# Kernel tuning notes

Measured on AMD Instinct MI355X. Metric: run time of the kernel, lower is better.

Reference implementation:

```python
import jax, jax.numpy as jnp
from jax import lax
import numpy as np

B, C_IN, H, W = 256, 2, 15, 15
DIM_MID, DIM_OUT = 128, 64
N_RES = 4  # DirectionalConvResBlocks

# tap positions inside a 3x3 kernel for each of the 4 line directions
# (matches DirectionalConvLayer.weight_func_map: horiz, vert, diag, anti-diag)
_POS = (((1, 0), (1, 1), (1, 2)),
        ((0, 1), (1, 1), (2, 1)),
        ((0, 0), (1, 1), (2, 2)),
        ((2, 0), (1, 1), (0, 2)))


def _dir_kernel(w3, d):
    # w3: [3, O, I] -> [O, I, 3, 3] with taps placed along direction d
    O, I = w3.shape[1], w3.shape[2]
    kern = jnp.zeros((O, I, 3, 3), w3.dtype)
    for k, (r, c) in enumerate(_POS[d]):
        kern = kern.at[:, :, r, c].set(w3[k])
    return kern


def _dconv(x, w3, b, d):
    kern = _dir_kernel(w3, d)
    y = lax.conv_general_dilated(x, kern, window_strides=(1, 1),
                                 padding=((1, 1), (1, 1)),
                                 dimension_numbers=('NCHW', 'OIHW', 'NCHW'))
    return y + b[None, :, None, None]


def _pw(x, w, b):
    # 1x1 conv: w [O, I]
    return jnp.einsum('bihw,oi->bohw', x, w) + b[None, :, None, None]


def setup_inputs() -> dict:
    key = jax.random.key(0)
    ks = jax.random.split(key, 16)
    s_in = 1.0 / np.sqrt(3 * C_IN)
    s_mid = 1.0 / np.sqrt(3 * DIM_MID)
    s_pw = 1.0 / np.sqrt(DIM_MID)
    return {
        'x': jax.random.normal(ks[0], (B, C_IN, H, W), jnp.float32),
        'dconv0_w': jax.random.normal(ks[1], (3, DIM_MID, C_IN), jnp.float32) * s_in,
        'dconv0_b': jnp.zeros((DIM_MID,), jnp.float32),
        'rb_dconv_w': jax.random.normal(ks[2], (N_RES, 3, DIM_MID, DIM_MID), jnp.float32) * s_mid,
        'rb_dconv_b': jnp.zeros((N_RES, DIM_MID), jnp.float32),
        'rb_c1_w': jax.random.normal(ks[3], (N_RES, DIM_MID, DIM_MID), jnp.float32) * s_pw,
        'rb_c1_b': jnp.zeros((N_RES, DIM_MID), jnp.float32),
        'c0_w1': jax.random.normal(ks[4], (DIM_MID, DIM_MID), jnp.float32) * s_pw,
        'c0_b1': jnp.zeros((DIM_MID,), jnp.float32),
        'c0_w2': jax.random.normal(ks[5], (DIM_MID, DIM_MID), jnp.float32) * s_pw,
        'c0_b2': jnp.zeros((DIM_MID,), jnp.float32),
        'final_w': jax.random.normal(ks[6], (DIM_OUT, DIM_MID), jnp.float32) * s_pw,
        'final_b': jnp.zeros((DIM_OUT,), jnp.float32),
    }


def reference(x, dconv0_w, dconv0_b, rb_dconv_w, rb_dconv_b, rb_c1_w, rb_c1_b,
              c0_w1, c0_b1, c0_w2, c0_b2, final_w, final_b):
    silu = jax.nn.silu
    outs = []
    for d in range(4):  # 4 board directions, shared weights
        h = silu(_dconv(x, dconv0_w, dconv0_b, d))
        for i in range(N_RES):  # DirectionalConvResBlock
            r = h
            h = silu(_dconv(h, rb_dconv_w[i], rb_dconv_b[i], d))
            h = silu(_pw(h, rb_c1_w[i], rb_c1_b[i]))
            h = h + r
        # Conv0dResBlock
        r = h
        h = silu(_pw(h, c0_w1, c0_b1))
        h = silu(_pw(h, c0_w2, c0_b2))
        h = h + r
        outs.append(_pw(h, final_w, final_b))
    return jnp.stack(outs, axis=1)  # [B, 4, DIM_OUT, H, W]
```

## Files before the change

kernel.cpp:

```cpp
#include <hip/hip_runtime.h>
#include <cstdint>
#include <cstddef>


#define HWX 15
#define NPOS 225
#define CH 128
#define NTH 256
#define ABYTES 8192
#define HOFF ABYTES
#define GRID_SLOTS 273
#define LDS_BYTES (ABYTES + GRID_SLOTS*256)
#define SAFE_PP 136

#define WSE_WDC 0
#define WSE_WC1 196608
#define WSE_W01 262144
#define WSE_W02 278528
#define WSE_WF  294912
#define WSE_TOTAL 303104
#define WS_NEED (WSE_TOTAL*2)

typedef _Float16 f16;
typedef __attribute__((ext_vector_type(8))) _Float16 f16x8;
typedef __attribute__((ext_vector_type(4))) _Float16 f16x4;
typedef __attribute__((ext_vector_type(4))) float f32x4;

__device__ __forceinline__ int hb_addr(int pp, int k){
  return HOFF + pp*256 + ((k*2) ^ ((pp&15)<<4));
}
__device__ __forceinline__ int a_addr(int o, int k){
  return o*64 + ((((k>>3))<<4) ^ ((o&3)<<4)) + ((k&7)*2);
}
__device__ __forceinline__ float silu_f(float v){ return v / (1.f + __expf(-v)); }

struct StReg { f16x8 a, b; bool on; };

template<bool WS>
__device__ __forceinline__ StReg stage_load(const f16* __restrict__ wsblk,
                                            const float* __restrict__ f32p,
                                            int stride, int rows, int tid){
  StReg r;
  const int o = tid>>1, kh = tid&1;
  r.on = (o < rows);
  if (r.on){
    if (WS){
      r.a = *(const f16x8*)(wsblk + o*32 + kh*16);
      r.b = *(const f16x8*)(wsblk + o*32 + kh*16 + 8);
    } else {
      const float* s = f32p + (size_t)o*stride + kh*16;
      float4 x0 = *(const float4*)(s);
      float4 x1 = *(const float4*)(s+4);
      float4 x2 = *(const float4*)(s+8);
      float4 x3 = *(const float4*)(s+12);
      r.a = (f16x8){(f16)x0.x,(f16)x0.y,(f16)x0.z,(f16)x0.w,
                    (f16)x1.x,(f16)x1.y,(f16)x1.z,(f16)x1.w};
      r.b = (f16x8){(f16)x2.x,(f16)x2.y,(f16)x2.z,(f16)x2.w,
                    (f16)x3.x,(f16)x3.y,(f16)x3.z,(f16)x3.w};
    }
  }
  return r;
}

__device__ __forceinline__ void stage_write(char* sm, StReg r, int tid){
  const int o = tid>>1, kh = tid&1;
  if (r.on){
    *(f16x8*)(sm + a_addr(o, kh*16))   = r.a;
    *(f16x8*)(sm + a_addr(o, kh*16+8)) = r.b;
  }
}

template<int MT>
__device__ __forceinline__ void gemm32(const char* sm, const int* pbs, int ks,
                                       int krow, int col, f32x4 acc[4][8]){
  const int kb = ks + krow*8;
  const int ka = krow*8;
  f16x8 b0 = *(const f16x8*)(sm + hb_addr(pbs[0], kb));
  f16x8 b1 = *(const f16x8*)(sm + hb_addr(pbs[1], kb));
  f16x8 b2 = *(const f16x8*)(sm + hb_addr(pbs[2], kb));
  f16x8 b3 = *(const f16x8*)(sm + hb_addr(pbs[3], kb));
#pragma unroll
  for (int mt=0; mt<MT; mt++){
    f16x8 a = *(const f16x8*)(sm + a_addr(mt*16+col, ka));
    acc[0][mt] = __builtin_amdgcn_mfma_f32_16x16x32_f16(a, b0, acc[0][mt], 0,0,0);
    acc[1][mt] = __builtin_amdgcn_mfma_f32_16x16x32_f16(a, b1, acc[1][mt], 0,0,0);
    acc[2][mt] = __builtin_amdgcn_mfma_f32_16x16x32_f16(a, b2, acc[2][mt], 0,0,0);
    acc[3][mt] = __builtin_amdgcn_mfma_f32_16x16x32_f16(a, b3, acc[3][mt], 0,0,0);
  }
}

template<int MT, bool WS>
__device__ __forceinline__ void pw_pass(char* sm, const f16* __restrict__ wsblk,
                                        const float* __restrict__ f32p,
                                        int stride, int rows, const int* pbs,
                                        int krow, int col, int tid, f32x4 acc[4][8]){
  StReg cur = stage_load<WS>(wsblk, f32p, stride, rows, tid);
#pragma unroll 1
  for (int ks=0; ks<CH; ks+=32){
    __syncthreads();
    stage_write(sm, cur, tid);
    if (ks+32 < CH)
      cur = stage_load<WS>(wsblk + (ks/32+1)*rows*32, f32p + ks + 32, stride, rows, tid);
    __syncthreads();
    gemm32<MT>(sm, pbs, ks, krow, col, acc);
  }
}

__device__ __forceinline__ void zacc_all(f32x4 acc[4][8]){
#pragma unroll
  for (int t=0;t<4;t++)
#pragma unroll
    for (int m=0;m<8;m++) acc[t][m] = (f32x4){0.f,0.f,0.f,0.f};
}

__device__ __forceinline__ void snap4x8(const char* sm, f16x4 r[4][8],
                                        const int* pbs, int krow){
#pragma unroll
  for (int t=0;t<4;t++)
#pragma unroll
    for (int mt=0;mt<8;mt++)
      r[t][mt] = *(const f16x4*)(sm + hb_addr(pbs[t], mt*16 + krow*4));
}

template<int MT, bool SILU, bool RES>
__device__ __forceinline__ void wb4(char* sm, f32x4 acc[4][8],
                                    const float* __restrict__ bias,
                                    f16x4 rsd[4][8], const int* pbs,
                                    const bool* val, int krow){
#pragma unroll
  for (int mt=0;mt<MT;mt++){
    const int ch0 = mt*16 + krow*4;
    float4 bb = *(const float4*)(bias + ch0);
    const float bj[4] = {bb.x, bb.y, bb.z, bb.w};
#pragma unroll
    for (int t=0;t<4;t++){
      f32x4 v = acc[t][mt];
#pragma unroll
      for (int j=0;j<4;j++) v[j] += bj[j];
      if (SILU){
#pragma unroll
        for (int j=0;j<4;j++) v[j] = silu_f(v[j]);
      }
      if (RES){
        f16x4 r = rsd[t][mt];
#pragma unroll
        for (int j=0;j<4;j++) v[j] += (float)r[j];
      }
      if (val[t]){
        f16x4 o = { (f16)v[0],(f16)v[1],(f16)v[2],(f16)v[3] };
        *(f16x4*)(sm + hb_addr(pbs[t], ch0)) = o;
      }
    }
  }
}

struct P {
  const float *x, *w0, *b0, *wdc, *bdc, *wc1, *bc1, *w01, *b01, *w02, *b02, *wf, *bf;
};

template<bool WS>
__global__ __launch_bounds__(NTH, 2)
void mix9_v3(const P p, const f16* __restrict__ wsf, float* __restrict__ out)
{
  __shared__ char sm[LDS_BYTES];
  const int tid  = threadIdx.x;
  const int lane = tid & 63;
  const int wave = tid >> 6;
  const int col  = lane & 15;
  const int krow = lane >> 4;
  const int d = blockIdx.x & 3;
  const int b = blockIdx.x >> 2;

  for (int i = tid; i < LDS_BYTES/16; i += NTH)
    ((f32x4*)sm)[i] = (f32x4){0.f,0.f,0.f,0.f};
  __syncthreads();

  for (int i = tid; i < 2*NPOS; i += NTH){
    const int ic = i/NPOS, n = i%NPOS;
    const int pp = (n/HWX + 1)*16 + (n%HWX + 1);
    *(f16*)(sm + hb_addr(pp, ic)) = (f16)p.x[(size_t)b*2*NPOS + i];
  }

  int pbs[4]; bool val[4];
#pragma unroll
  for (int t=0;t<4;t++){
    const int r = wave*4 + t;
    val[t] = (col >= 1) && (r < HWX);
    pbs[t] = val[t] ? (r+1)*16 + col : SAFE_PP;
  }
  int dneg;
  switch (d){
    case 0:  dneg = -1;  break;
    case 1:  dneg = -16; break;
    case 2:  dneg = -17; break;
    default: dneg =  15; break;
  }

  f32x4 acc[4][8];
  f16x4 rsd[4][8];

  zacc_all(acc);
#pragma unroll 1
  for (int k=0;k<3;k++){
    const int sh = (k==0) ? dneg : (k==1) ? 0 : -dneg;
    int pbt[4];
#pragma unroll
    for (int t=0;t<4;t++) pbt[t] = pbs[t] + sh;
    __syncthreads();
    *(f16*)(sm + a_addr(tid>>1, tid&1)) = (f16)p.w0[k*256 + tid];
    __syncthreads();
    gemm32<8>(sm, pbt, 0, krow, col, acc);
  }
  __syncthreads();
  wb4<8,true,false>(sm, acc, p.b0, nullptr, pbs, val, krow);

#pragma unroll 1
  for (int res=0; res<4; res++){
    zacc_all(acc);
#pragma unroll 1
    for (int k=0;k<3;k++){
      const int sh = (k==0) ? dneg : (k==1) ? 0 : -dneg;
      int pbt[4];
#pragma unroll
      for (int t=0;t<4;t++) pbt[t] = pbs[t] + sh;
      const f16* blk = wsf + WSE_WDC + (size_t)(res*3 + k)*4*4096;
      const float* fp = p.wdc + (size_t)(res*3 + k)*CH*CH;
      pw_pass<8,WS>(sm, blk, fp, CH, CH, pbt, krow, col, tid, acc);
    }
    __syncthreads();
    snap4x8(sm, rsd, pbs, krow);
    wb4<8,true,false>(sm, acc, p.bdc + res*CH, nullptr, pbs, val, krow);

    zacc_all(acc);
    pw_pass<8,WS>(sm, wsf + WSE_WC1 + (size_t)res*4*4096,
                  p.wc1 + (size_t)res*CH*CH, CH, CH, pbs, krow, col, tid, acc);
    __syncthreads();
    wb4<8,true,true>(sm, acc, p.bc1 + res*CH, rsd, pbs, val, krow);
  }

  zacc_all(acc);
  pw_pass<8,WS>(sm, wsf + WSE_W01, p.w01, CH, CH, pbs, krow, col, tid, acc);
  __syncthreads();
  snap4x8(sm, rsd, pbs, krow);
  wb4<8,true,false>(sm, acc, p.b01, nullptr, pbs, val, krow);

  zacc_all(acc);
  pw_pass<8,WS>(sm, wsf + WSE_W02, p.w02, CH, CH, pbs, krow, col, tid, acc);
  __syncthreads();
  wb4<8,true,true>(sm, acc, p.b02, rsd, pbs, val, krow);

  zacc_all(acc);
  pw_pass<4,WS>(sm, wsf + WSE_WF, p.wf, CH, 64, pbs, krow, col, tid, acc);

  float* ob = out + ((size_t)(b*4 + d)*64)*NPOS;
#pragma unroll
  for (int t=0;t<4;t++){
    const int r = wave*4 + t;
    const int n = r*HWX + (col-1);
#pragma unroll
    for (int mt=0;mt<4;mt++){
      const int ch0 = mt*16 + krow*4;
      float4 bb = *(const float4*)(p.bf + ch0);
      const float bj[4] = {bb.x, bb.y, bb.z, bb.w};
#pragma unroll
      for (int j=0;j<4;j++)
        if (val[t]) ob[(size_t)(ch0+j)*NPOS + n] = acc[t][mt][j] + bj[j];
    }
  }
}

__global__ void cvt_ws(const P p, f16* __restrict__ ws)
{
  const int idx = blockIdx.x*NTH + threadIdx.x;
  if (idx >= WSE_TOTAL) return;
  float v;
  if (idx < WSE_WC1){
    int blk = idx >> 12, rem = idx & 4095;
    int o = rem >> 5, k = rem & 31;
    int ks = blk & 3, tapres = blk >> 2;
    v = p.wdc[((size_t)tapres*CH + o)*CH + ks*32 + k];
  } else if (idx < WSE_W01){
    int j = idx - WSE_WC1;
    int blk = j >> 12, rem = j & 4095;
    int o = rem >> 5, k = rem & 31;
    int ks = blk & 3, res = blk >> 2;
    v = p.wc1[((size_t)res*CH + o)*CH + ks*32 + k];
  } else if (idx < WSE_W02){
    int j = idx - WSE_W01;
    int ks = j >> 12, rem = j & 4095;
    int o = rem >> 5, k = rem & 31;
    v = p.w01[(size_t)o*CH + ks*32 + k];
  } else if (idx < WSE_WF){
    int j = idx - WSE_W02;
    int ks = j >> 12, rem = j & 4095;
    int o = rem >> 5, k = rem & 31;
    v = p.w02[(size_t)o*CH + ks*32 + k];
  } else {
    int j = idx - WSE_WF;
    int ks = j >> 11, rem = j & 2047;
    int o = rem >> 5, k = rem & 31;
    v = p.wf[(size_t)o*CH + ks*32 + k];
  }
  ws[idx] = (f16)v;
}

extern "C" void kernel_launch(void* const* d_in, const int* in_sizes, int n_in,
                              void* d_out, int out_size, void* d_ws, size_t ws_size,
                              hipStream_t stream)
{
  (void)in_sizes; (void)n_in; (void)out_size;
  P p;
  p.x   = (const float*)d_in[0];
  p.w0  = (const float*)d_in[1];
  p.b0  = (const float*)d_in[2];
  p.wdc = (const float*)d_in[3];
  p.bdc = (const float*)d_in[4];
  p.wc1 = (const float*)d_in[5];
  p.bc1 = (const float*)d_in[6];
  p.w01 = (const float*)d_in[7];
  p.b01 = (const float*)d_in[8];
  p.w02 = (const float*)d_in[9];
  p.b02 = (const float*)d_in[10];
  p.wf  = (const float*)d_in[11];
  p.bf  = (const float*)d_in[12];

  float* out = (float*)d_out;
  const bool ws_ok = (d_ws != nullptr) && (ws_size >= (size_t)WS_NEED);

  if (ws_ok){
    f16* ws = (f16*)d_ws;
    cvt_ws<<<dim3((WSE_TOTAL + NTH - 1)/NTH), dim3(NTH), 0, stream>>>(p, ws);
    mix9_v3<true><<<dim3(256*4), dim3(NTH), 0, stream>>>(p, ws, out);
  } else {
    mix9_v3<false><<<dim3(256*4), dim3(NTH), 0, stream>>>(p, nullptr, out);
  }
}
```

Before: 518.5 us.

## Load MFMA weight fragments directly from global memory instead of LDS staging

Drops the LDS A-operand staging buffer and the two barriers per k-slice. Each wave now reads its f16 weight fragments straight from the pre-converted workspace (L2/L1 cached) inside the MFMA loop. The first-layer weights are pre-packed into the workspace as zero-padded tiles, and output is staged through LDS so the global stores are coalesced float4 writes. This trades LDS traffic and barrier stalls for redundant global/cache loads across the four waves, and adds a few barriers around the writebacks.

After: 975.5 us. 1.88x slower.

```diff
diff --git a/kernel.cpp b/kernel.cpp
--- a/kernel.cpp
+++ b/kernel.cpp
@@ -7,10 +7,8 @@
 #define NPOS 225
 #define CH 128
 #define NTH 256
-#define ABYTES 8192
-#define HOFF ABYTES
 #define GRID_SLOTS 273
-#define LDS_BYTES (ABYTES + GRID_SLOTS*256)
+#define LDS_BYTES (GRID_SLOTS*256)
 #define SAFE_PP 136
 
 #define WSE_WDC 0
@@ -18,7 +16,8 @@
 #define WSE_W01 262144
 #define WSE_W02 278528
 #define WSE_WF  294912
-#define WSE_TOTAL 303104
+#define WSE_W0  303104
+#define WSE_TOTAL 315392
 #define WS_NEED (WSE_TOTAL*2)
 
 typedef _Float16 f16;
@@ -27,61 +26,32 @@
 typedef __attribute__((ext_vector_type(4))) float f32x4;
 
 __device__ __forceinline__ int hb_addr(int pp, int k){
-  return HOFF + pp*256 + ((k*2) ^ ((pp&15)<<4));
-}
-__device__ __forceinline__ int a_addr(int o, int k){
-  return o*64 + ((((k>>3))<<4) ^ ((o&3)<<4)) + ((k&7)*2);
+  return pp*256 + ((k*2) ^ ((pp&15)<<4));
 }
 __device__ __forceinline__ float silu_f(float v){ return v / (1.f + __expf(-v)); }
 
-struct StReg { f16x8 a, b; bool on; };
-
-template<bool WS>
-__device__ __forceinline__ StReg stage_load(const f16* __restrict__ wsblk,
-                                            const float* __restrict__ f32p,
-                                            int stride, int rows, int tid){
-  StReg r;
-  const int o = tid>>1, kh = tid&1;
-  r.on = (o < rows);
-  if (r.on){
+template<int MT, bool WS>
+__device__ __forceinline__ void gemm_k32(const char* sm, const f16* __restrict__ wsblk,
+    const float* __restrict__ f32w, const int* pbt, int ksabs, int krow, int col,
+    f32x4 acc[4][8]){
+  const int kb = ksabs + krow*8;
+  const int k8 = krow*8;
+  f16x8 b0 = *(const f16x8*)(sm + hb_addr(pbt[0], kb));
+  f16x8 b1 = *(const f16x8*)(sm + hb_addr(pbt[1], kb));
+  f16x8 b2 = *(const f16x8*)(sm + hb_addr(pbt[2], kb));
+  f16x8 b3 = *(const f16x8*)(sm + hb_addr(pbt[3], kb));
+#pragma unroll
+  for (int mt=0; mt<MT; mt++){
+    const int o = mt*16 + col;
+    f16x8 a;
     if (WS){
-      r.a = *(const f16x8*)(wsblk + o*32 + kh*16);
-      r.b = *(const f16x8*)(wsblk + o*32 + kh*16 + 8);
+      a = *(const f16x8*)(wsblk + o*32 + k8);
     } else {
-      const float* s = f32p + (size_t)o*stride + kh*16;
-      float4 x0 = *(const float4*)(s);
-      float4 x1 = *(const float4*)(s+4);
-      float4 x2 = *(const float4*)(s+8);
-      float4 x3 = *(const float4*)(s+12);
-      r.a = (f16x8){(f16)x0.x,(f16)x0.y,(f16)x0.z,(f16)x0.w,
-                    (f16)x1.x,(f16)x1.y,(f16)x1.z,(f16)x1.w};
-      r.b = (f16x8){(f16)x2.x,(f16)x2.y,(f16)x2.z,(f16)x2.w,
-                    (f16)x3.x,(f16)x3.y,(f16)x3.z,(f16)x3.w};
-    }
-  }
-  return r;
-}
-
-__device__ __forceinline__ void stage_write(char* sm, StReg r, int tid){
-  const int o = tid>>1, kh = tid&1;
-  if (r.on){
-    *(f16x8*)(sm + a_addr(o, kh*16))   = r.a;
-    *(f16x8*)(sm + a_addr(o, kh*16+8)) = r.b;
-  }
-}
-
-template<int MT>
-__device__ __forceinline__ void gemm32(const char* sm, const int* pbs, int ks,
-                                       int krow, int col, f32x4 acc[4][8]){
-  const int kb = ks + krow*8;
-  const int ka = krow*8;
-  f16x8 b0 = *(const f16x8*)(sm + hb_addr(pbs[0], kb));
-  f16x8 b1 = *(const f16x8*)(sm + hb_addr(pbs[1], kb));
-  f16x8 b2 = *(const f16x8*)(sm + hb_addr(pbs[2], kb));
-  f16x8 b3 = *(const f16x8*)(sm + hb_addr(pbs[3], kb));
-#pragma unroll
-  for (int mt=0; mt<MT; mt++){
-    f16x8 a = *(const f16x8*)(sm + a_addr(mt*16+col, ka));
+      const float* s = f32w + (size_t)o*CH + ksabs + k8;
+      float4 x0 = *(const float4*)(s), x1 = *(const float4*)(s+4);
+      a = (f16x8){(f16)x0.x,(f16)x0.y,(f16)x0.z,(f16)x0.w,
+                  (f16)x1.x,(f16)x1.y,(f16)x1.z,(f16)x1.w};
+    }
     acc[0][mt] = __builtin_amdgcn_mfma_f32_16x16x32_f16(a, b0, acc[0][mt], 0,0,0);
     acc[1][mt] = __builtin_amdgcn_mfma_f32_16x16x32_f16(a, b1, acc[1][mt], 0,0,0);
     acc[2][mt] = __builtin_amdgcn_mfma_f32_16x16x32_f16(a, b2, acc[2][mt], 0,0,0);
@@ -90,19 +60,39 @@
 }
 
 template<int MT, bool WS>
-__device__ __forceinline__ void pw_pass(char* sm, const f16* __restrict__ wsblk,
-                                        const float* __restrict__ f32p,
-                                        int stride, int rows, const int* pbs,
-                                        int krow, int col, int tid, f32x4 acc[4][8]){
-  StReg cur = stage_load<WS>(wsblk, f32p, stride, rows, tid);
-#pragma unroll 1
-  for (int ks=0; ks<CH; ks+=32){
-    __syncthreads();
-    stage_write(sm, cur, tid);
-    if (ks+32 < CH)
-      cur = stage_load<WS>(wsblk + (ks/32+1)*rows*32, f32p + ks + 32, stride, rows, tid);
-    __syncthreads();
-    gemm32<MT>(sm, pbs, ks, krow, col, acc);
+__device__ __forceinline__ void pass128(const char* sm, const f16* __restrict__ wsbase,
+    int blkElems, const float* __restrict__ f32w, const int* pbt, int krow, int col,
+    f32x4 acc[4][8]){
+#pragma unroll
+  for (int kq=0; kq<4; kq++)
+    gemm_k32<MT,WS>(sm, wsbase + (size_t)kq*blkElems, f32w, pbt, kq*32, krow, col, acc);
+}
+
+template<bool WS>
+__device__ __forceinline__ void gemm_l0(const char* sm, const f16* __restrict__ wsblk,
+    const float* __restrict__ w0tap, const int* pbt, int krow, int col, f32x4 acc[4][8]){
+  const int kb = krow*8;
+  f16x8 b0 = *(const f16x8*)(sm + hb_addr(pbt[0], kb));
+  f16x8 b1 = *(const f16x8*)(sm + hb_addr(pbt[1], kb));
+  f16x8 b2 = *(const f16x8*)(sm + hb_addr(pbt[2], kb));
+  f16x8 b3 = *(const f16x8*)(sm + hb_addr(pbt[3], kb));
+#pragma unroll
+  for (int mt=0; mt<8; mt++){
+    const int o = mt*16 + col;
+    f16x8 a;
+    if (WS){
+      a = *(const f16x8*)(wsblk + o*32 + kb);
+    } else {
+      a = (f16x8){(f16)0,(f16)0,(f16)0,(f16)0,(f16)0,(f16)0,(f16)0,(f16)0};
+      if (krow == 0){
+        float2 w = *(const float2*)(w0tap + o*2);
+        a[0] = (f16)w.x; a[1] = (f16)w.y;
+      }
+    }
+    acc[0][mt] = __builtin_amdgcn_mfma_f32_16x16x32_f16(a, b0, acc[0][mt], 0,0,0);
+    acc[1][mt] = __builtin_amdgcn_mfma_f32_16x16x32_f16(a, b1, acc[1][mt], 0,0,0);
+    acc[2][mt] = __builtin_amdgcn_mfma_f32_16x16x32_f16(a, b2, acc[2][mt], 0,0,0);
+    acc[3][mt] = __builtin_amdgcn_mfma_f32_16x16x32_f16(a, b3, acc[3][mt], 0,0,0);
   }
 }
 
@@ -160,7 +150,7 @@
 
 template<bool WS>
 __global__ __launch_bounds__(NTH, 2)
-void mix9_v3(const P p, const f16* __restrict__ wsf, float* __restrict__ out)
+void mix9_v4(const P p, const f16* __restrict__ wsf, float* __restrict__ out)
 {
   __shared__ char sm[LDS_BYTES];
   const int tid  = threadIdx.x;
@@ -180,6 +170,7 @@
     const int pp = (n/HWX + 1)*16 + (n%HWX + 1);
     *(f16*)(sm + hb_addr(pp, ic)) = (f16)p.x[(size_t)b*2*NPOS + i];
   }
+  __syncthreads();
 
   int pbs[4]; bool val[4];
 #pragma unroll
@@ -206,13 +197,12 @@
     int pbt[4];
 #pragma unroll
     for (int t=0;t<4;t++) pbt[t] = pbs[t] + sh;
-    __syncthreads();
-    *(f16*)(sm + a_addr(tid>>1, tid&1)) = (f16)p.w0[k*256 + tid];
-    __syncthreads();
-    gemm32<8>(sm, pbt, 0, krow, col, acc);
+    gemm_l0<WS>(sm, wsf + WSE_W0 + (size_t)k*4096, p.w0 + (size_t)k*CH*2,
+                pbt, krow, col, acc);
   }
   __syncthreads();
   wb4<8,true,false>(sm, acc, p.b0, nullptr, pbs, val, krow);
+  __syncthreads();
 
 #pragma unroll 1
   for (int res=0; res<4; res++){
@@ -223,50 +213,60 @@
       int pbt[4];
 #pragma unroll
       for (int t=0;t<4;t++) pbt[t] = pbs[t] + sh;
-      const f16* blk = wsf + WSE_WDC + (size_t)(res*3 + k)*4*4096;
-      const float* fp = p.wdc + (size_t)(res*3 + k)*CH*CH;
-      pw_pass<8,WS>(sm, blk, fp, CH, CH, pbt, krow, col, tid, acc);
+      pass128<8,WS>(sm, wsf + WSE_WDC + (size_t)(res*3+k)*4*4096, 4096,
+                    p.wdc + (size_t)(res*3+k)*CH*CH, pbt, krow, col, acc);
     }
     __syncthreads();
     snap4x8(sm, rsd, pbs, krow);
     wb4<8,true,false>(sm, acc, p.bdc + res*CH, nullptr, pbs, val, krow);
+    __syncthreads();
 
     zacc_all(acc);
-    pw_pass<8,WS>(sm, wsf + WSE_WC1 + (size_t)res*4*4096,
-                  p.wc1 + (size_t)res*CH*CH, CH, CH, pbs, krow, col, tid, acc);
+    pass128<8,WS>(sm, wsf + WSE_WC1 + (size_t)res*4*4096, 4096,
+                  p.wc1 + (size_t)res*CH*CH, pbs, krow, col, acc);
     __syncthreads();
     wb4<8,true,true>(sm, acc, p.bc1 + res*CH, rsd, pbs, val, krow);
+    __syncthreads();
   }
 
   zacc_all(acc);
-  pw_pass<8,WS>(sm, wsf + WSE_W01, p.w01, CH, CH, pbs, krow, col, tid, acc);
+  pass128<8,WS>(sm, wsf + WSE_W01, 4096, p.w01, pbs, krow, col, acc);
   __syncthreads();
   snap4x8(sm, rsd, pbs, krow);
   wb4<8,true,false>(sm, acc, p.b01, nullptr, pbs, val, krow);
+  __syncthreads();
 
   zacc_all(acc);
-  pw_pass<8,WS>(sm, wsf + WSE_W02, p.w02, CH, CH, pbs, krow, col, tid, acc);
+  pass128<8,WS>(sm, wsf + WSE_W02, 4096, p.w02, pbs, krow, col, acc);
   __syncthreads();
   wb4<8,true,true>(sm, acc, p.b02, rsd, pbs, val, krow);
+  __syncthreads();
 
   zacc_all(acc);
-  pw_pass<4,WS>(sm, wsf + WSE_WF, p.wf, CH, 64, pbs, krow, col, tid, acc);
-
-  float* ob = out + ((size_t)(b*4 + d)*64)*NPOS;
+  pass128<4,WS>(sm, wsf + WSE_WF, 2048, p.wf, pbs, krow, col, acc);
+  __syncthreads();
+
+  float* osm = (float*)sm;
 #pragma unroll
   for (int t=0;t<4;t++){
-    const int r = wave*4 + t;
-    const int n = r*HWX + (col-1);
-#pragma unroll
-    for (int mt=0;mt<4;mt++){
-      const int ch0 = mt*16 + krow*4;
-      float4 bb = *(const float4*)(p.bf + ch0);
-      const float bj[4] = {bb.x, bb.y, bb.z, bb.w};
-#pragma unroll
-      for (int j=0;j<4;j++)
-        if (val[t]) ob[(size_t)(ch0+j)*NPOS + n] = acc[t][mt][j] + bj[j];
-    }
-  }
+    if (val[t]){
+      const int r = wave*4 + t;
+      const int n = r*HWX + (col-1);
+#pragma unroll
+      for (int mt=0;mt<4;mt++){
+        const int ch0 = mt*16 + krow*4;
+        float4 bb = *(const float4*)(p.bf + ch0);
+        osm[(ch0+0)*NPOS + n] = acc[t][mt][0] + bb.x;
+        osm[(ch0+1)*NPOS + n] = acc[t][mt][1] + bb.y;
+        osm[(ch0+2)*NPOS + n] = acc[t][mt][2] + bb.z;
+        osm[(ch0+3)*NPOS + n] = acc[t][mt][3] + bb.w;
+      }
+    }
+  }
+  __syncthreads();
+  float* ob = out + (size_t)(b*4 + d)*64*NPOS;
+  for (int i = tid; i < (64*NPOS)/4; i += NTH)
+    *(float4*)(ob + i*4) = *(const float4*)(osm + i*4);
 }
 
 __global__ void cvt_ws(const P p, f16* __restrict__ ws)
@@ -295,11 +295,16 @@
     int ks = j >> 12, rem = j & 4095;
     int o = rem >> 5, k = rem & 31;
     v = p.w02[(size_t)o*CH + ks*32 + k];
-  } else {
+  } else if (idx < WSE_W0){
     int j = idx - WSE_WF;
     int ks = j >> 11, rem = j & 2047;
     int o = rem >> 5, k = rem & 31;
     v = p.wf[(size_t)o*CH + ks*32 + k];
+  } else {
+    int j = idx - WSE_W0;
+    int tap = j >> 12, rem = j & 4095;
+    int o = rem >> 5, k = rem & 31;
+    v = (k < 2) ? p.w0[((size_t)tap*CH + o)*2 + k] : 0.f;
   }
   ws[idx] = (f16)v;
 }
@@ -330,8 +335,8 @@
   if (ws_ok){
     f16* ws = (f16*)d_ws;
     cvt_ws<<<dim3((WSE_TOTAL + NTH - 1)/NTH), dim3(NTH), 0, stream>>>(p, ws);
-    mix9_v3<true><<<dim3(256*4), dim3(NTH), 0, stream>>>(p, ws, out);
+    mix9_v4<true><<<dim3(256*4), dim3(NTH), 0, stream>>>(p, ws, out);
   } else {
-    mix9_v3<false><<<dim3(256*4), dim3(NTH), 0, stream>>>(p, nullptr, out);
-  }
-}
+    mix9_v4<false><<<dim3(256*4), dim3(NTH), 0, stream>>>(p, nullptr, out);
+  }
+}
```
